# Optimization experiments

Measured on AMD Instinct MI355X. Metric: run time of the kernel, lower is better.

## Reference

```python
import jax, jax.numpy as jnp
import numpy as np

B, S, H, F, E, TOP_K = 4, 2048, 1024, 4096, 8, 2


def setup_inputs() -> dict:
    key = jax.random.key(0)
    ks = jax.random.split(key, 5)
    scale = 0.02
    return {
        "hidden_states": jax.random.normal(ks[0], (B, S, H), dtype=jnp.float32),
        "router_w": jax.random.normal(ks[1], (E, H), dtype=jnp.float32) * scale,
        "gate_w": jax.random.normal(ks[2], (E, F, H), dtype=jnp.float32) * scale,
        "up_w": jax.random.normal(ks[3], (E, F, H), dtype=jnp.float32) * scale,
        "down_w": jax.random.normal(ks[4], (E, H, F), dtype=jnp.float32) * scale,
    }


def reference(hidden_states, router_w, gate_w, up_w, down_w):
    b, s, h = hidden_states.shape
    x = hidden_states.reshape(-1, h)                        # [T, H]
    router_logits = x @ router_w.T                          # [T, E]
    routing_weights = jax.nn.softmax(router_logits.astype(jnp.float32), axis=-1)
    top_k_weights, top_k_index = jax.lax.top_k(routing_weights, TOP_K)
    top_k_weights = top_k_weights.astype(x.dtype)           # NOTE: Jamba does NOT renormalize
    # dense combine weights: [T, E], zero where expert not selected
    w_full = jnp.sum(
        jax.nn.one_hot(top_k_index, E, dtype=x.dtype) * top_k_weights[..., None], axis=1
    )

    def expert_step(acc, ew):
        gw, uw, dw, w = ew                                  # [F,H], [F,H], [H,F], [T]
        hid = jax.nn.silu(x @ gw.T) * (x @ uw.T)            # [T, F]
        return acc + w[:, None] * (hid @ dw.T), None

    out0 = jnp.zeros_like(x)
    out, _ = jax.lax.scan(expert_step, out0, (gate_w, up_w, down_w, w_full.T))
    return out.reshape(b, s, h)
```

## Files before the change

### kernel.cpp

```cpp
#include <hip/hip_runtime.h>
#include <hip/hip_bf16.h>


#define T_TOKENS 8192
#define H_DIM    1024
#define F_DIM    4096
#define E_NUM    8
#define NSLOT_CAP 17408
#define MAX_TILES 136

typedef __attribute__((ext_vector_type(8))) __bf16 bf16x8;
typedef __attribute__((ext_vector_type(4))) float  floatx4;
typedef __attribute__((ext_vector_type(8))) unsigned short ushort8;

__device__ __forceinline__ unsigned short f2bf(float f) {
    unsigned int u = __builtin_bit_cast(unsigned int, f);
    u += 0x7fffu + ((u >> 16) & 1u);
    return (unsigned short)(u >> 16);
}

__device__ __forceinline__ void stage16(const void* g, void* l) {
    __builtin_amdgcn_global_load_lds(
        (const __attribute__((address_space(1))) void*)g,
        (__attribute__((address_space(3))) void*)l, 16, 0, 0);
}

__global__ __launch_bounds__(256) void router_kernel(
    const float* __restrict__ x, const float* __restrict__ rw,
    int* __restrict__ topk_id, float* __restrict__ topk_w, int* __restrict__ counts)
{
    __shared__ float s_rw[E_NUM * H_DIM];
    int tid = threadIdx.x;
    for (int i = tid; i < E_NUM * H_DIM; i += 256) s_rw[i] = rw[i];
    __syncthreads();
    int wave = tid >> 6, lane = tid & 63;
    int token = blockIdx.x * 4 + wave;
    const float* xr = x + (size_t)token * H_DIM;
    float acc[E_NUM];
#pragma unroll
    for (int e = 0; e < E_NUM; e++) acc[e] = 0.f;
    for (int k = lane; k < H_DIM; k += 64) {
        float xv = xr[k];
#pragma unroll
        for (int e = 0; e < E_NUM; e++) acc[e] += xv * s_rw[e * H_DIM + k];
    }
#pragma unroll
    for (int e = 0; e < E_NUM; e++) {
        float v = acc[e];
#pragma unroll
        for (int off = 32; off > 0; off >>= 1) v += __shfl_xor(v, off, 64);
        acc[e] = v;
    }
    if (lane == 0) {
        float mx = acc[0];
#pragma unroll
        for (int e = 1; e < E_NUM; e++) mx = fmaxf(mx, acc[e]);
        float p[E_NUM]; float sum = 0.f;
#pragma unroll
        for (int e = 0; e < E_NUM; e++) { p[e] = __expf(acc[e] - mx); sum += p[e]; }
        float inv = 1.f / sum;
        int i0 = 0; float v0 = p[0];
#pragma unroll
        for (int e = 1; e < E_NUM; e++) if (p[e] > v0) { v0 = p[e]; i0 = e; }
        int i1 = -1; float v1 = -1.f;
#pragma unroll
        for (int e = 0; e < E_NUM; e++) if (e != i0 && p[e] > v1) { v1 = p[e]; i1 = e; }
        topk_id[token * 2] = i0;     topk_w[token * 2] = v0 * inv;
        topk_id[token * 2 + 1] = i1; topk_w[token * 2 + 1] = v1 * inv;
        atomicAdd(&counts[i0], 1);   atomicAdd(&counts[i1], 1);
    }
}

__global__ void plan_kernel(const int* __restrict__ counts, int* __restrict__ offs,
                            int* __restrict__ tile_expert, int* __restrict__ tile_row)
{
    if (threadIdx.x == 0 && blockIdx.x == 0) {
        int off = 0, t = 0;
        for (int e = 0; e < E_NUM; e++) {
            offs[e] = off;
            int nt = (counts[e] + 127) >> 7;
            for (int i = 0; i < nt; i++) { tile_expert[t] = e; tile_row[t] = off + i * 128; t++; }
            off += nt * 128;
        }
        offs[E_NUM] = off;
        for (; t < MAX_TILES; t++) { tile_expert[t] = -1; tile_row[t] = 0; }
    }
}

__global__ __launch_bounds__(256) void scatter_kernel(
    const int* __restrict__ topk_id, const float* __restrict__ topk_w,
    const int* __restrict__ offs, int* __restrict__ fill,
    int* __restrict__ token_list, float* __restrict__ w_list)
{
    int i = blockIdx.x * 256 + threadIdx.x;
    if (i < T_TOKENS * 2) {
        int e = topk_id[i];
        int pos = atomicAdd(&fill[e], 1);
        int slot = offs[e] + pos;
        token_list[slot] = i >> 1;
        w_list[slot] = topk_w[i];
    }
}

__global__ __launch_bounds__(256) void cvt_x_kernel(
    const float* __restrict__ x, unsigned short* __restrict__ xb)
{
    int i = (blockIdx.x * 256 + threadIdx.x) * 4;
    float4 v = *(const float4*)(x + i);
    ushort4 o;
    o.x = f2bf(v.x); o.y = f2bf(v.y); o.z = f2bf(v.z); o.w = f2bf(v.w);
    *(ushort4*)(xb + i) = o;
}

__global__ __launch_bounds__(256, 2) void gateup_kernel(
    const unsigned short* __restrict__ xb, const float* __restrict__ gate_w,
    const float* __restrict__ up_w, const int* __restrict__ token_list,
    const int* __restrict__ tile_expert, const int* __restrict__ tile_row,
    unsigned short* __restrict__ hid)
{
    int e = tile_expert[blockIdx.y];
    if (e < 0) return;
    int m0 = tile_row[blockIdx.y];
    int n0 = blockIdx.x * 128;

    __shared__ unsigned short As[128 * 32];
    __shared__ unsigned short Bg[128 * 32];
    __shared__ unsigned short Bu[128 * 32];

    int tid = threadIdx.x;
    int wave = tid >> 6, lane = tid & 63;

    int arow0 = wave * 16 + (lane >> 2);
    int aseg  = lane & 3;
    int tok0 = token_list[m0 + arow0];
    int tok1 = token_list[m0 + 64 + arow0];
    const unsigned short* ap0 = xb + (size_t)tok0 * H_DIM + aseg * 8;
    const unsigned short* ap1 = xb + (size_t)tok1 * H_DIM + aseg * 8;
    unsigned short* al0 = As + wave * 512;
    unsigned short* al1 = As + 2048 + wave * 512;

    int brow = tid >> 1, bhalf = tid & 1;
    const float* gp = gate_w + ((size_t)e * F_DIM + n0 + brow) * H_DIM + bhalf * 16;
    const float* upp = up_w  + ((size_t)e * F_DIM + n0 + brow) * H_DIM + bhalf * 16;
    int bofs = brow * 32 + bhalf * 16;

    int wm = (wave & 1) * 64, wn = (wave >> 1) * 64;
    int lrow = lane & 15, lquad = lane >> 4;

    floatx4 accg[4][4], accu[4][4];
#pragma unroll
    for (int i = 0; i < 4; i++)
#pragma unroll
        for (int j = 0; j < 4; j++) {
            accg[i][j] = (floatx4){0.f, 0.f, 0.f, 0.f};
            accu[i][j] = (floatx4){0.f, 0.f, 0.f, 0.f};
        }

    for (int kt = 0; kt < H_DIM / 32; kt++) {
        const float* gk = gp + kt * 32;
        const float* uk = upp + kt * 32;
        float4 g0 = *(const float4*)(gk);      float4 g1 = *(const float4*)(gk + 4);
        float4 g2 = *(const float4*)(gk + 8);  float4 g3 = *(const float4*)(gk + 12);
        float4 u0 = *(const float4*)(uk);      float4 u1 = *(const float4*)(uk + 4);
        float4 u2 = *(const float4*)(uk + 8);  float4 u3 = *(const float4*)(uk + 12);

        __syncthreads();

        stage16(ap0 + kt * 32, al0);
        stage16(ap1 + kt * 32, al1);

        ushort8 p0, p1, q0, q1;
        p0[0]=f2bf(g0.x); p0[1]=f2bf(g0.y); p0[2]=f2bf(g0.z); p0[3]=f2bf(g0.w);
        p0[4]=f2bf(g1.x); p0[5]=f2bf(g1.y); p0[6]=f2bf(g1.z); p0[7]=f2bf(g1.w);
        p1[0]=f2bf(g2.x); p1[1]=f2bf(g2.y); p1[2]=f2bf(g2.z); p1[3]=f2bf(g2.w);
        p1[4]=f2bf(g3.x); p1[5]=f2bf(g3.y); p1[6]=f2bf(g3.z); p1[7]=f2bf(g3.w);
        q0[0]=f2bf(u0.x); q0[1]=f2bf(u0.y); q0[2]=f2bf(u0.z); q0[3]=f2bf(u0.w);
        q0[4]=f2bf(u1.x); q0[5]=f2bf(u1.y); q0[6]=f2bf(u1.z); q0[7]=f2bf(u1.w);
        q1[0]=f2bf(u2.x); q1[1]=f2bf(u2.y); q1[2]=f2bf(u2.z); q1[3]=f2bf(u2.w);
        q1[4]=f2bf(u3.x); q1[5]=f2bf(u3.y); q1[6]=f2bf(u3.z); q1[7]=f2bf(u3.w);
        *(ushort8*)(&Bg[bofs]) = p0;  *(ushort8*)(&Bg[bofs + 8]) = p1;
        *(ushort8*)(&Bu[bofs]) = q0;  *(ushort8*)(&Bu[bofs + 8]) = q1;

        __syncthreads();

        bf16x8 af[4], bgf[4], buf2[4];
#pragma unroll
        for (int mi = 0; mi < 4; mi++)
            af[mi] = *(const bf16x8*)(&As[(wm + mi * 16 + lrow) * 32 + lquad * 8]);
#pragma unroll
        for (int ni = 0; ni < 4; ni++) {
            bgf[ni]  = *(const bf16x8*)(&Bg[(wn + ni * 16 + lrow) * 32 + lquad * 8]);
            buf2[ni] = *(const bf16x8*)(&Bu[(wn + ni * 16 + lrow) * 32 + lquad * 8]);
        }
#pragma unroll
        for (int mi = 0; mi < 4; mi++)
#pragma unroll
            for (int ni = 0; ni < 4; ni++) {
                accg[mi][ni] = __builtin_amdgcn_mfma_f32_16x16x32_bf16(af[mi], bgf[ni],  accg[mi][ni], 0, 0, 0);
                accu[mi][ni] = __builtin_amdgcn_mfma_f32_16x16x32_bf16(af[mi], buf2[ni], accu[mi][ni], 0, 0, 0);
            }
    }

#pragma unroll
    for (int mi = 0; mi < 4; mi++)
#pragma unroll
        for (int r = 0; r < 4; r++) {
            size_t srow = (size_t)(m0 + wm + mi * 16 + lquad * 4 + r);
            unsigned short* hrow = hid + srow * F_DIM + n0 + wn + lrow;
#pragma unroll
            for (int ni = 0; ni < 4; ni++) {
                float g = accg[mi][ni][r];
                float u = accu[mi][ni][r];
                float sg = __builtin_amdgcn_rcpf(1.f + __expf(-g));
                hrow[ni * 16] = f2bf(g * sg * u);
            }
        }
}

__global__ __launch_bounds__(256, 2) void down_kernel(
    const unsigned short* __restrict__ hid, const float* __restrict__ down_w,
    const int* __restrict__ token_list, const float* __restrict__ w_list,
    const int* __restrict__ tile_expert, const int* __restrict__ tile_row,
    float* __restrict__ out)
{
    int e = tile_expert[blockIdx.y];
    if (e < 0) return;
    int m0 = tile_row[blockIdx.y];
    int n0 = blockIdx.x * 128;

    __shared__ unsigned short As[128 * 32];
    __shared__ unsigned short Bs[128 * 32];

    int tid = threadIdx.x;
    int wave = tid >> 6, lane = tid & 63;

    int arow0 = wave * 16 + (lane >> 2);
    int aseg  = lane & 3;
    const unsigned short* ap0 = hid + (size_t)(m0 + arow0) * F_DIM + aseg * 8;
    const unsigned short* ap1 = hid + (size_t)(m0 + 64 + arow0) * F_DIM + aseg * 8;
    unsigned short* al0 = As + wave * 512;
    unsigned short* al1 = As + 2048 + wave * 512;

    int brow = tid >> 1, bhalf = tid & 1;
    const float* bp = down_w + ((size_t)e * H_DIM + n0 + brow) * F_DIM + bhalf * 16;
    int bofs = brow * 32 + bhalf * 16;

    int wm = (wave & 1) * 64, wn = (wave >> 1) * 64;
    int lrow = lane & 15, lquad = lane >> 4;

    floatx4 acc[4][4];
#pragma unroll
    for (int i = 0; i < 4; i++)
#pragma unroll
        for (int j = 0; j < 4; j++) acc[i][j] = (floatx4){0.f, 0.f, 0.f, 0.f};

    for (int kt = 0; kt < F_DIM / 32; kt++) {
        const float* bk = bp + kt * 32;
        float4 b0 = *(const float4*)(bk);      float4 b1 = *(const float4*)(bk + 4);
        float4 b2 = *(const float4*)(bk + 8);  float4 b3 = *(const float4*)(bk + 12);

        __syncthreads();

        stage16(ap0 + kt * 32, al0);
        stage16(ap1 + kt * 32, al1);

        ushort8 p0, p1;
        p0[0]=f2bf(b0.x); p0[1]=f2bf(b0.y); p0[2]=f2bf(b0.z); p0[3]=f2bf(b0.w);
        p0[4]=f2bf(b1.x); p0[5]=f2bf(b1.y); p0[6]=f2bf(b1.z); p0[7]=f2bf(b1.w);
        p1[0]=f2bf(b2.x); p1[1]=f2bf(b2.y); p1[2]=f2bf(b2.z); p1[3]=f2bf(b2.w);
        p1[4]=f2bf(b3.x); p1[5]=f2bf(b3.y); p1[6]=f2bf(b3.z); p1[7]=f2bf(b3.w);
        *(ushort8*)(&Bs[bofs]) = p0;  *(ushort8*)(&Bs[bofs + 8]) = p1;

        __syncthreads();

        bf16x8 af[4], bf[4];
#pragma unroll
        for (int mi = 0; mi < 4; mi++)
            af[mi] = *(const bf16x8*)(&As[(wm + mi * 16 + lrow) * 32 + lquad * 8]);
#pragma unroll
        for (int ni = 0; ni < 4; ni++)
            bf[ni] = *(const bf16x8*)(&Bs[(wn + ni * 16 + lrow) * 32 + lquad * 8]);
#pragma unroll
        for (int mi = 0; mi < 4; mi++)
#pragma unroll
            for (int ni = 0; ni < 4; ni++)
                acc[mi][ni] = __builtin_amdgcn_mfma_f32_16x16x32_bf16(af[mi], bf[ni], acc[mi][ni], 0, 0, 0);
    }

#pragma unroll
    for (int mi = 0; mi < 4; mi++)
#pragma unroll
        for (int r = 0; r < 4; r++) {
            int slot = m0 + wm + mi * 16 + lquad * 4 + r;
            int tok = token_list[slot];
            float w = w_list[slot];
            float* orow = out + (size_t)tok * H_DIM + n0 + wn + lrow;
#pragma unroll
            for (int ni = 0; ni < 4; ni++)
                atomicAdd(&orow[ni * 16], w * acc[mi][ni][r]);
        }
}

extern "C" void kernel_launch(void* const* d_in, const int* in_sizes, int n_in,
                              void* d_out, int out_size, void* d_ws, size_t ws_size,
                              hipStream_t stream) {
    (void)in_sizes; (void)n_in;
    const float* x        = (const float*)d_in[0];
    const float* router_w = (const float*)d_in[1];
    const float* gate_w   = (const float*)d_in[2];
    const float* up_w     = (const float*)d_in[3];
    const float* down_w   = (const float*)d_in[4];
    float* out = (float*)d_out;

    char* ws = (char*)d_ws;
    size_t off = 0;
    unsigned short* xb  = (unsigned short*)(ws + off); off += (size_t)T_TOKENS * H_DIM * 2;
    unsigned short* hid = (unsigned short*)(ws + off); off += (size_t)NSLOT_CAP * F_DIM * 2;
    int*   topk_id = (int*)(ws + off);   off += T_TOKENS * 2 * 4;
    float* topk_w  = (float*)(ws + off); off += T_TOKENS * 2 * 4;
    char* zbase = ws + off;
    int*   token_list = (int*)(ws + off);   off += NSLOT_CAP * 4;
    float* w_list     = (float*)(ws + off); off += NSLOT_CAP * 4;
    int* counts = (int*)(ws + off); off += 32;
    int* offs   = (int*)(ws + off); off += 64;
    int* fill   = (int*)(ws + off); off += 32;
    int* tile_expert = (int*)(ws + off); off += 576;
    int* tile_row    = (int*)(ws + off); off += 576;
    if (off > ws_size) return;

    hipMemsetAsync(zbase, 0, (size_t)((ws + off) - zbase), stream);
    hipMemsetAsync(d_out, 0, (size_t)out_size * 4, stream);

    cvt_x_kernel  <<<(T_TOKENS * H_DIM / 4) / 256, 256, 0, stream>>>(x, xb);
    router_kernel <<<T_TOKENS / 4, 256, 0, stream>>>(x, router_w, topk_id, topk_w, counts);
    plan_kernel   <<<1, 1, 0, stream>>>(counts, offs, tile_expert, tile_row);
    scatter_kernel<<<(T_TOKENS * 2) / 256, 256, 0, stream>>>(topk_id, topk_w, offs, fill, token_list, w_list);
    gateup_kernel <<<dim3(F_DIM / 128, MAX_TILES), 256, 0, stream>>>(
        xb, gate_w, up_w, token_list, tile_expert, tile_row, hid);
    down_kernel   <<<dim3(H_DIM / 128, MAX_TILES), 256, 0, stream>>>(
        hid, down_w, token_list, w_list, tile_expert, tile_row, out);
}
```

Baseline: 1.487 ms.

## Pre-convert expert weights to bf16 and stage all GEMM operands via direct LDS loads

```diff
diff --git a/kernel.cpp b/kernel.cpp
--- a/kernel.cpp
+++ b/kernel.cpp
@@ -112,6 +112,183 @@
     *(ushort4*)(xb + i) = o;
 }
 
+__global__ __launch_bounds__(256) void cvt_w_kernel(
+    const float* __restrict__ src, unsigned short* __restrict__ dst)
+{
+    size_t i = ((size_t)blockIdx.x * 256 + threadIdx.x) * 4;
+    float4 v = *(const float4*)(src + i);
+    ushort4 o;
+    o.x = f2bf(v.x); o.y = f2bf(v.y); o.z = f2bf(v.z); o.w = f2bf(v.w);
+    *(ushort4*)(dst + i) = o;
+}
+
+
+__global__ __launch_bounds__(256, 4) void gateup_bf16_kernel(
+    const unsigned short* __restrict__ xb, const unsigned short* __restrict__ gwb,
+    const unsigned short* __restrict__ uwb, const int* __restrict__ token_list,
+    const int* __restrict__ tile_expert, const int* __restrict__ tile_row,
+    unsigned short* __restrict__ hid)
+{
+    int e = tile_expert[blockIdx.y];
+    if (e < 0) return;
+    int m0 = tile_row[blockIdx.y];
+    int n0 = blockIdx.x * 64;
+
+    __shared__ unsigned short As[128 * 32];
+    __shared__ unsigned short Bg[64 * 32];
+    __shared__ unsigned short Bu[64 * 32];
+
+    int tid = threadIdx.x;
+    int wave = tid >> 6, lane = tid & 63;
+    int r16 = lane >> 2;
+    int seg = (lane & 3) ^ ((lane >> 3) & 3);
+
+    int tok0 = token_list[m0 + wave * 16 + r16];
+    int tok1 = token_list[m0 + 64 + wave * 16 + r16];
+    const unsigned short* ap0 = xb + (size_t)tok0 * H_DIM + seg * 8;
+    const unsigned short* ap1 = xb + (size_t)tok1 * H_DIM + seg * 8;
+    unsigned short* al0 = As + wave * 512;
+    unsigned short* al1 = As + 2048 + wave * 512;
+
+    size_t brow = (size_t)e * F_DIM + n0 + wave * 16 + r16;
+    const unsigned short* gp = gwb + brow * H_DIM + seg * 8;
+    const unsigned short* up = uwb + brow * H_DIM + seg * 8;
+    unsigned short* bgl = Bg + wave * 512;
+    unsigned short* bul = Bu + wave * 512;
+
+    int wm = (wave & 1) * 64, wn = (wave >> 1) * 32;
+    int lrow = lane & 15, lquad = lane >> 4;
+    int pq = (lquad ^ ((lrow >> 1) & 3)) * 8;
+
+    floatx4 accg[4][2], accu[4][2];
+#pragma unroll
+    for (int i = 0; i < 4; i++)
+#pragma unroll
+        for (int j = 0; j < 2; j++) {
+            accg[i][j] = (floatx4){0.f, 0.f, 0.f, 0.f};
+            accu[i][j] = (floatx4){0.f, 0.f, 0.f, 0.f};
+        }
+
+    for (int kt = 0; kt < H_DIM / 32; kt++) {
+        int ko = kt * 32;
+        __syncthreads();
+        stage16(ap0 + ko, al0);
+        stage16(ap1 + ko, al1);
+        stage16(gp + ko, bgl);
+        stage16(up + ko, bul);
+        __syncthreads();
+
+        bf16x8 af[4], bgf[2], buf2[2];
+#pragma unroll
+        for (int mi = 0; mi < 4; mi++)
+            af[mi] = *(const bf16x8*)(&As[(wm + mi * 16 + lrow) * 32 + pq]);
+#pragma unroll
+        for (int ni = 0; ni < 2; ni++) {
+            bgf[ni]  = *(const bf16x8*)(&Bg[(wn + ni * 16 + lrow) * 32 + pq]);
+            buf2[ni] = *(const bf16x8*)(&Bu[(wn + ni * 16 + lrow) * 32 + pq]);
+        }
+#pragma unroll
+        for (int mi = 0; mi < 4; mi++)
+#pragma unroll
+            for (int ni = 0; ni < 2; ni++) {
+                accg[mi][ni] = __builtin_amdgcn_mfma_f32_16x16x32_bf16(af[mi], bgf[ni],  accg[mi][ni], 0, 0, 0);
+                accu[mi][ni] = __builtin_amdgcn_mfma_f32_16x16x32_bf16(af[mi], buf2[ni], accu[mi][ni], 0, 0, 0);
+            }
+    }
+
+#pragma unroll
+    for (int mi = 0; mi < 4; mi++)
+#pragma unroll
+        for (int r = 0; r < 4; r++) {
+            size_t srow = (size_t)(m0 + wm + mi * 16 + lquad * 4 + r);
+            unsigned short* hrow = hid + srow * F_DIM + n0 + wn + lrow;
+#pragma unroll
+            for (int ni = 0; ni < 2; ni++) {
+                float g = accg[mi][ni][r];
+                float u = accu[mi][ni][r];
+                float sg = __builtin_amdgcn_rcpf(1.f + __expf(-g));
+                hrow[ni * 16] = f2bf(g * sg * u);
+            }
+        }
+}
+
+__global__ __launch_bounds__(256, 3) void down_bf16_kernel(
+    const unsigned short* __restrict__ hid, const unsigned short* __restrict__ dwb,
+    const int* __restrict__ token_list, const float* __restrict__ w_list,
+    const int* __restrict__ tile_expert, const int* __restrict__ tile_row,
+    float* __restrict__ out)
+{
+    int e = tile_expert[blockIdx.y];
+    if (e < 0) return;
+    int m0 = tile_row[blockIdx.y];
+    int n0 = blockIdx.x * 128;
+
+    __shared__ unsigned short As[128 * 32];
+    __shared__ unsigned short Bs[128 * 32];
+
+    int tid = threadIdx.x;
+    int wave = tid >> 6, lane = tid & 63;
+    int r16 = lane >> 2;
+    int seg = (lane & 3) ^ ((lane >> 3) & 3);
+
+    const unsigned short* ap0 = hid + (size_t)(m0 + wave * 16 + r16) * F_DIM + seg * 8;
+    const unsigned short* ap1 = hid + (size_t)(m0 + 64 + wave * 16 + r16) * F_DIM + seg * 8;
+    unsigned short* al0 = As + wave * 512;
+    unsigned short* al1 = As + 2048 + wave * 512;
+
+    size_t brow = (size_t)e * H_DIM + n0 + wave * 16 + r16;
+    const unsigned short* bp0 = dwb + brow * F_DIM + seg * 8;
+    const unsigned short* bp1 = dwb + (brow + 64) * F_DIM + seg * 8;
+    unsigned short* bl0 = Bs + wave * 512;
+    unsigned short* bl1 = Bs + 2048 + wave * 512;
+
+    int wm = (wave & 1) * 64, wn = (wave >> 1) * 64;
+    int lrow = lane & 15, lquad = lane >> 4;
+    int pq = (lquad ^ ((lrow >> 1) & 3)) * 8;
+
+    floatx4 acc[4][4];
+#pragma unroll
+    for (int i = 0; i < 4; i++)
+#pragma unroll
+        for (int j = 0; j < 4; j++) acc[i][j] = (floatx4){0.f, 0.f, 0.f, 0.f};
+
+    for (int kt = 0; kt < F_DIM / 32; kt++) {
+        int ko = kt * 32;
+        __syncthreads();
+        stage16(ap0 + ko, al0);
+        stage16(ap1 + ko, al1);
+        stage16(bp0 + ko, bl0);
+        stage16(bp1 + ko, bl1);
+        __syncthreads();
+
+        bf16x8 af[4], bf[4];
+#pragma unroll
+        for (int mi = 0; mi < 4; mi++)
+            af[mi] = *(const bf16x8*)(&As[(wm + mi * 16 + lrow) * 32 + pq]);
+#pragma unroll
+        for (int ni = 0; ni < 4; ni++)
+            bf[ni] = *(const bf16x8*)(&Bs[(wn + ni * 16 + lrow) * 32 + pq]);
+#pragma unroll
+        for (int mi = 0; mi < 4; mi++)
+#pragma unroll
+            for (int ni = 0; ni < 4; ni++)
+                acc[mi][ni] = __builtin_amdgcn_mfma_f32_16x16x32_bf16(af[mi], bf[ni], acc[mi][ni], 0, 0, 0);
+    }
+
+#pragma unroll
+    for (int mi = 0; mi < 4; mi++)
+#pragma unroll
+        for (int r = 0; r < 4; r++) {
+            int slot = m0 + wm + mi * 16 + lquad * 4 + r;
+            int tok = token_list[slot];
+            float w = w_list[slot];
+            float* orow = out + (size_t)tok * H_DIM + n0 + wn + lrow;
+#pragma unroll
+            for (int ni = 0; ni < 4; ni++)
+                atomicAdd(&orow[ni * 16], w * acc[mi][ni][r]);
+        }
+}
+
 __global__ __launch_bounds__(256, 2) void gateup_kernel(
     const unsigned short* __restrict__ xb, const float* __restrict__ gate_w,
     const float* __restrict__ up_w, const int* __restrict__ token_list,
@@ -165,7 +342,6 @@
         float4 u2 = *(const float4*)(uk + 8);  float4 u3 = *(const float4*)(uk + 12);
 
         __syncthreads();
-
         stage16(ap0 + kt * 32, al0);
         stage16(ap1 + kt * 32, al1);
 
@@ -260,7 +436,6 @@
         float4 b2 = *(const float4*)(bk + 8);  float4 b3 = *(const float4*)(bk + 12);
 
         __syncthreads();
-
         stage16(ap0 + kt * 32, al0);
         stage16(ap1 + kt * 32, al1);
 
@@ -311,6 +486,8 @@
     const float* up_w     = (const float*)d_in[3];
     const float* down_w   = (const float*)d_in[4];
     float* out = (float*)d_out;
+
+    const size_t W_ELEMS = (size_t)E_NUM * F_DIM * H_DIM;
 
     char* ws = (char*)d_ws;
     size_t off = 0;
@@ -326,17 +503,35 @@
     int* fill   = (int*)(ws + off); off += 32;
     int* tile_expert = (int*)(ws + off); off += 576;
     int* tile_row    = (int*)(ws + off); off += 576;
-    if (off > ws_size) return;
-
-    hipMemsetAsync(zbase, 0, (size_t)((ws + off) - zbase), stream);
+    size_t zend = off;
+    off = (off + 255) & ~(size_t)255;
+    unsigned short* gwb = (unsigned short*)(ws + off); off += W_ELEMS * 2;
+    unsigned short* uwb = (unsigned short*)(ws + off); off += W_ELEMS * 2;
+    unsigned short* dwb = gwb;
+    bool big_ws = (off <= ws_size);
+    if (zend > ws_size) return;
+
+    hipMemsetAsync(zbase, 0, (size_t)((ws + zend) - zbase), stream);
     hipMemsetAsync(d_out, 0, (size_t)out_size * 4, stream);
 
     cvt_x_kernel  <<<(T_TOKENS * H_DIM / 4) / 256, 256, 0, stream>>>(x, xb);
     router_kernel <<<T_TOKENS / 4, 256, 0, stream>>>(x, router_w, topk_id, topk_w, counts);
     plan_kernel   <<<1, 1, 0, stream>>>(counts, offs, tile_expert, tile_row);
     scatter_kernel<<<(T_TOKENS * 2) / 256, 256, 0, stream>>>(topk_id, topk_w, offs, fill, token_list, w_list);
-    gateup_kernel <<<dim3(F_DIM / 128, MAX_TILES), 256, 0, stream>>>(
-        xb, gate_w, up_w, token_list, tile_expert, tile_row, hid);
-    down_kernel   <<<dim3(H_DIM / 128, MAX_TILES), 256, 0, stream>>>(
-        hid, down_w, token_list, w_list, tile_expert, tile_row, out);
-}
+
+    if (big_ws) {
+        int wblocks = (int)(W_ELEMS / 4 / 256);
+        cvt_w_kernel<<<wblocks, 256, 0, stream>>>(gate_w, gwb);
+        cvt_w_kernel<<<wblocks, 256, 0, stream>>>(up_w, uwb);
+        gateup_bf16_kernel<<<dim3(F_DIM / 64, MAX_TILES), 256, 0, stream>>>(
+            xb, gwb, uwb, token_list, tile_expert, tile_row, hid);
+        cvt_w_kernel<<<wblocks, 256, 0, stream>>>(down_w, dwb);
+        down_bf16_kernel<<<dim3(H_DIM / 128, MAX_TILES), 256, 0, stream>>>(
+            hid, dwb, token_list, w_list, tile_expert, tile_row, out);
+    } else {
+        gateup_kernel<<<dim3(F_DIM / 128, MAX_TILES), 256, 0, stream>>>(
+            xb, gate_w, up_w, token_list, tile_expert, tile_row, hid);
+        down_kernel<<<dim3(H_DIM / 128, MAX_TILES), 256, 0, stream>>>(
+            hid, down_w, token_list, w_list, tile_expert, tile_row, out);
+    }
+}
```

New measurement: 1.296 ms. -12.8%, faster.
